# Optimization experiments

Hardware: AMD Instinct MI355X
Metric: run time of the kernel (lower is better)

Reference implementation:

```python
import jax, jax.numpy as jnp
import numpy as np

N_NODES = 50000
N_EDGES = 65536
D_NODE = 1024
D_HID = 1024


def setup_inputs() -> dict:
    key = jax.random.key(0)
    k1, k2, k3, k4, k5 = jax.random.split(key, 5)
    node_feats = jax.random.normal(k1, (N_NODES, D_NODE), dtype=jnp.float32)
    src = jax.random.randint(k2, (N_EDGES,), 0, N_NODES, dtype=jnp.int64)
    dst = jax.random.randint(k3, (N_EDGES,), 0, N_NODES, dtype=jnp.int64)
    # MLP([2048, 1024, 1024]) with ReLU between layers, bias, no BN, no dropout
    W1 = jax.random.normal(k4, (2 * D_NODE, D_HID), dtype=jnp.float32) * (1.0 / np.sqrt(2 * D_NODE))
    b1 = jnp.zeros((D_HID,), dtype=jnp.float32)
    W2 = jax.random.normal(k5, (D_HID, D_HID), dtype=jnp.float32) * (1.0 / np.sqrt(D_HID))
    b2 = jnp.zeros((D_HID,), dtype=jnp.float32)
    return {"node_feats": node_feats, "src": src, "dst": dst,
            "W1": W1, "b1": b1, "W2": W2, "b2": b2}


def reference(node_feats, src, dst, W1, b1, W2, b2):
    # gather per-edge src/dst node features and concat: [E, 2d]
    feat = jnp.concatenate([node_feats[src], node_feats[dst]], axis=1)
    # edge MLP: Linear -> ReLU -> Linear
    h = jax.nn.relu(feat @ W1 + b1)
    e_f = h @ W2 + b2  # [E, D_HID]
    return e_f
```

## Files before the change

### kernel.cpp

```cpp
#include <hip/hip_runtime.h>
#include <stdint.h>
#include <stddef.h>

typedef unsigned short u16;
typedef __bf16 bf16_t;
typedef bf16_t bf16x8 __attribute__((ext_vector_type(8)));
typedef float f32x4 __attribute__((ext_vector_type(4)));
typedef u16 u16x4 __attribute__((ext_vector_type(4)));

#define N_NODES 50000
#define N_EDGES 65536
#define D_NODE 1024
#define D_HID 1024

#define BM 256
#define BK 64
#define BUFE (BM * BK)
#define LDS_BYTES (4 * BUFE * 2)


__device__ __forceinline__ u16 f2bf(float f) {
  union { float f; uint32_t u; } v; v.f = f;
  uint32_t u = v.u;
  u += 0x7FFF + ((u >> 16) & 1);
  return (u16)(u >> 16);
}

typedef __attribute__((address_space(1))) const void GV;
typedef __attribute__((address_space(3))) void LV;

__device__ __forceinline__ void gll16(const void* g, void* lds_wave_base) {
  __builtin_amdgcn_global_load_lds((GV*)g, (LV*)lds_wave_base, 16, 0, 0);
}


__global__ void detect_i64_kernel(const int* __restrict__ src, int* __restrict__ flag) {
  if (threadIdx.x == 0 && blockIdx.x == 0) {
    int o = 0;
    for (int i = 1; i < 32; i += 2) o |= src[i];
    *flag = (o == 0) ? 1 : 0;
  }
}

__global__ void cvt_bf16_kernel(const float* __restrict__ in, u16* __restrict__ out, size_t n4) {
  size_t i = (size_t)blockIdx.x * blockDim.x + threadIdx.x;
  if (i >= n4) return;
  float4 v = reinterpret_cast<const float4*>(in)[i];
  u16x4 o;
  o.x = f2bf(v.x); o.y = f2bf(v.y); o.z = f2bf(v.z); o.w = f2bf(v.w);
  reinterpret_cast<u16x4*>(out)[i] = o;
}

__global__ void transpose_cvt_kernel(const float* __restrict__ in, u16* __restrict__ out,
                                     int K, int N) {
  __shared__ float tile[32][33];
  int n0 = blockIdx.x * 32, k0 = blockIdx.y * 32;
  int tx = threadIdx.x, ty = threadIdx.y;
  #pragma unroll
  for (int i = ty; i < 32; i += 8)
    tile[i][tx] = in[(size_t)(k0 + i) * N + (n0 + tx)];
  __syncthreads();
  #pragma unroll
  for (int i = ty; i < 32; i += 8)
    out[(size_t)(n0 + i) * K + (k0 + tx)] = f2bf(tile[tx][i]);
}


template <bool FIRST>
__device__ __forceinline__ void gemm_body(const u16* __restrict__ Abf,
                                          const int* __restrict__ src,
                                          const int* __restrict__ dst,
                                          const int* __restrict__ is64p,
                                          const u16* __restrict__ Bt,
                                          const float* __restrict__ bias,
                                          u16* __restrict__ hout,
                                          float* __restrict__ fout,
                                          const int K) {
  extern __shared__ __align__(16) u16 lds[];
  u16* const ldsA = lds;
  u16* const ldsB = lds + 2 * BUFE;

  const int t = threadIdx.x;
  const int lane = t & 63;
  const int wave = t >> 6;

  const int b = blockIdx.x;
  const int wgid = (b & 7) * 128 + (b >> 3);
  const int bm = (wgid >> 2) * BM;
  const int bn = (wgid & 3) * BM;

  const int wm = (wave >> 2) * 128;
  const int wn = (wave & 3) * 64;

  const int srow = t >> 3;
  const int kswz = (((t & 7) ^ (srow & 7)) << 3);
  const int stoff = wave * 512;

  const u16* ap[4];
  const u16* ad[4];
  const u16* bp[4];
  if constexpr (FIRST) {
    const int is64 = *is64p;
    #pragma unroll
    for (int q = 0; q < 4; ++q) {
      const int e = bm + q * 64 + srow;
      const int s = is64 ? src[2 * e] : src[e];
      const int d = is64 ? dst[2 * e] : dst[e];
      ap[q] = Abf + (size_t)s * D_NODE + kswz;
      ad[q] = Abf + (size_t)d * D_NODE + kswz;
    }
  } else {
    #pragma unroll
    for (int q = 0; q < 4; ++q) {
      ap[q] = Abf + (size_t)(bm + q * 64 + srow) * K + kswz;
      ad[q] = nullptr;
    }
  }
  #pragma unroll
  for (int q = 0; q < 4; ++q)
    bp[q] = Bt + (size_t)(bn + q * 64 + srow) * K + kswz;

  auto stageA = [&](int buf, int q, int u) {
    const u16* g;
    if constexpr (FIRST) {
      g = (u < (D_NODE / BK)) ? (ap[q] + u * BK) : (ad[q] + (u - D_NODE / BK) * BK);
    } else {
      g = ap[q] + u * BK;
    }
    gll16(g, ldsA + buf * BUFE + q * 4096 + stoff);
  };
  auto stageB = [&](int buf, int q, int u) {
    gll16(bp[q] + u * BK, ldsB + buf * BUFE + q * 4096 + stoff);
  };
  auto stageGroup = [&](int buf, int u) {
    stageA(buf, 0, u); stageA(buf, 1, u); stageA(buf, 2, u); stageA(buf, 3, u);
    stageB(buf, 0, u); stageB(buf, 1, u); stageB(buf, 2, u); stageB(buf, 3, u);
  };

  const int lm = lane & 15;
  const int kq8 = ((lane >> 4) & 3) << 3;
  const int swzr = (lm & 7) << 3;
  const int kb0 = kq8 ^ swzr;
  const int kb1 = (32 + kq8) ^ swzr;
  const int arow = (wm + lm) * BK;
  const int brow = (wn + lm) * BK;

  f32x4 acc[8][4] = {};

  const int NT = K / BK;

  stageGroup(0, 0);
  stageGroup(1, 1);
  asm volatile("s_waitcnt vmcnt(8)" ::: "memory");
  __builtin_amdgcn_s_barrier();

  for (int u = 0; u < NT; ++u) {
    const int cb = u & 1;
    const u16* As_c = ldsA + cb * BUFE;
    const u16* Bs_c = ldsB + cb * BUFE;

    bf16x8 aq[4], ar[4], bq[4], br[4];

    #pragma unroll
    for (int j = 0; j < 4; ++j)
      bq[j] = *reinterpret_cast<const bf16x8*>(Bs_c + brow + j * 1024 + kb0);
    #pragma unroll
    for (int i = 0; i < 4; ++i)
      aq[i] = *reinterpret_cast<const bf16x8*>(As_c + arow + i * 1024 + kb0);
    #pragma unroll
    for (int i = 0; i < 4; ++i)
      ar[i] = *reinterpret_cast<const bf16x8*>(As_c + arow + (i + 4) * 1024 + kb0);

    __builtin_amdgcn_s_setprio(1);
    #pragma unroll
    for (int i = 0; i < 4; ++i)
      #pragma unroll
      for (int j = 0; j < 4; ++j)
        acc[i][j] = __builtin_amdgcn_mfma_f32_16x16x32_bf16(aq[i], bq[j], acc[i][j], 0, 0, 0);
    __builtin_amdgcn_s_setprio(0);

    #pragma unroll
    for (int j = 0; j < 4; ++j)
      br[j] = *reinterpret_cast<const bf16x8*>(Bs_c + brow + j * 1024 + kb1);
    bf16x8 aq2[4];
    #pragma unroll
    for (int i = 0; i < 4; ++i)
      aq2[i] = *reinterpret_cast<const bf16x8*>(As_c + arow + i * 1024 + kb1);
    bf16x8 ar2[4];
    #pragma unroll
    for (int i = 0; i < 4; ++i)
      ar2[i] = *reinterpret_cast<const bf16x8*>(As_c + arow + (i + 4) * 1024 + kb1);

    __builtin_amdgcn_s_setprio(1);
    #pragma unroll
    for (int i = 0; i < 4; ++i)
      #pragma unroll
      for (int j = 0; j < 4; ++j)
        acc[i + 4][j] = __builtin_amdgcn_mfma_f32_16x16x32_bf16(ar[i], bq[j], acc[i + 4][j], 0, 0, 0);
    __builtin_amdgcn_s_setprio(0);

    asm volatile("s_waitcnt lgkmcnt(0)" ::: "memory");
    __builtin_amdgcn_sched_barrier(0);
    __builtin_amdgcn_s_barrier();
    __builtin_amdgcn_sched_barrier(0);

    if (u + 2 < NT) stageGroup(cb, u + 2);

    __builtin_amdgcn_s_setprio(1);
    #pragma unroll
    for (int i = 0; i < 4; ++i)
      #pragma unroll
      for (int j = 0; j < 4; ++j)
        acc[i][j] = __builtin_amdgcn_mfma_f32_16x16x32_bf16(aq2[i], br[j], acc[i][j], 0, 0, 0);
    #pragma unroll
    for (int i = 0; i < 4; ++i)
      #pragma unroll
      for (int j = 0; j < 4; ++j)
        acc[i + 4][j] = __builtin_amdgcn_mfma_f32_16x16x32_bf16(ar2[i], br[j], acc[i + 4][j], 0, 0, 0);
    __builtin_amdgcn_s_setprio(0);

    if (u + 2 < NT)      asm volatile("s_waitcnt vmcnt(8)" ::: "memory");
    else if (u + 1 < NT) asm volatile("s_waitcnt vmcnt(0)" ::: "memory");
    __builtin_amdgcn_s_barrier();
  }

  const int rq = ((lane >> 4) & 3) * 4;
  #pragma unroll
  for (int j = 0; j < 4; ++j) {
    const int n = bn + wn + 16 * j + lm;
    const float bj = bias[n];
    #pragma unroll
    for (int i = 0; i < 8; ++i) {
      const int m0 = bm + wm + 16 * i + rq;
      f32x4 c = acc[i][j];
      #pragma unroll
      for (int rr = 0; rr < 4; ++rr) {
        float vv = c[rr] + bj;
        if (FIRST) {
          vv = fmaxf(vv, 0.0f);
          hout[(size_t)(m0 + rr) * D_HID + n] = f2bf(vv);
        } else {
          fout[(size_t)(m0 + rr) * D_HID + n] = vv;
        }
      }
    }
  }
}

__launch_bounds__(512, 2)
__global__ void gemm1_kernel(const u16* __restrict__ Abf, const int* __restrict__ src,
                             const int* __restrict__ dst, const int* __restrict__ is64p,
                             const u16* __restrict__ Bt, const float* __restrict__ bias,
                             u16* __restrict__ hout) {
  gemm_body<true>(Abf, src, dst, is64p, Bt, bias, hout, nullptr, 2 * D_NODE);
}

__launch_bounds__(512, 2)
__global__ void gemm2_kernel(const u16* __restrict__ Abf, const u16* __restrict__ Bt,
                             const float* __restrict__ bias, float* __restrict__ fout) {
  gemm_body<false>(Abf, nullptr, nullptr, nullptr, Bt, bias, nullptr, fout, D_HID);
}


extern "C" void kernel_launch(void* const* d_in, const int* in_sizes, int n_in,
                              void* d_out, int out_size, void* d_ws, size_t ws_size,
                              hipStream_t stream) {
  const float* node_feats = (const float*)d_in[0];
  const int*   src        = (const int*)d_in[1];
  const int*   dst        = (const int*)d_in[2];
  const float* W1         = (const float*)d_in[3];
  const float* b1         = (const float*)d_in[4];
  const float* W2         = (const float*)d_in[5];
  const float* b2         = (const float*)d_in[6];
  float* out = (float*)d_out;

  u16* ws = (u16*)d_ws;
  const size_t NODE_E = (size_t)N_NODES * D_NODE;
  u16* node_bf = ws;
  u16* W1T = node_bf + NODE_E;
  u16* W2T = W1T + (size_t)2048 * 1024;
  u16* h   = W2T + (size_t)1024 * 1024;
  int* flag = (int*)(h + (size_t)N_EDGES * D_HID);

  static bool attr_set = false;
  if (!attr_set) {
    hipFuncSetAttribute(reinterpret_cast<const void*>(&gemm1_kernel),
                        hipFuncAttributeMaxDynamicSharedMemorySize, LDS_BYTES);
    hipFuncSetAttribute(reinterpret_cast<const void*>(&gemm2_kernel),
                        hipFuncAttributeMaxDynamicSharedMemorySize, LDS_BYTES);
    attr_set = true;
  }

  detect_i64_kernel<<<1, 64, 0, stream>>>(src, flag);

  cvt_bf16_kernel<<<(unsigned)(NODE_E / 4 / 256), 256, 0, stream>>>(node_feats, node_bf, NODE_E / 4);

  transpose_cvt_kernel<<<dim3(1024 / 32, 2048 / 32), dim3(32, 8), 0, stream>>>(W1, W1T, 2048, 1024);
  transpose_cvt_kernel<<<dim3(1024 / 32, 1024 / 32), dim3(32, 8), 0, stream>>>(W2, W2T, 1024, 1024);

  gemm1_kernel<<<1024, 512, LDS_BYTES, stream>>>(node_bf, src, dst, flag, W1T, b1, h);

  gemm2_kernel<<<1024, 512, LDS_BYTES, stream>>>(h, W2T, b2, out);
}
```

Baseline: 804.5 us.

## Switch GEMMs to 4-wave blocks with 128x128 per-wave tiles and simpler double buffering

Each workgroup now runs 256 threads (4 waves), and each wave computes a 128x128 output tile with an 8x8 accumulator array instead of 128x64 with 8 waves. The hand-tuned two-stage prefetch with split barriers and setprio is replaced by a plain double buffer: prefetch the next tile at the top of the loop, then __syncthreads at the end. Global addressing switches to 32-bit byte offsets to save registers. The larger register tile raises MFMA reuse per LDS load, but it needs many more VGPRs, and occupancy drops to one block per CU, so latency hiding relies on the single prefetch stage.

```diff
diff --git a/kernel.cpp b/kernel.cpp
--- a/kernel.cpp
+++ b/kernel.cpp
@@ -89,144 +89,108 @@
   const int bm = (wgid >> 2) * BM;
   const int bn = (wgid & 3) * BM;
 
-  const int wm = (wave >> 2) * 128;
-  const int wn = (wave & 3) * 64;
-
-  const int srow = t >> 3;
-  const int kswz = (((t & 7) ^ (srow & 7)) << 3);
-  const int stoff = wave * 512;
-
-  const u16* ap[4];
-  const u16* ad[4];
-  const u16* bp[4];
+  const int wm = (wave >> 1) * 128;
+  const int wn = (wave & 1) * 128;
+
+  const int srb = t >> 3;
+  const int kswz = (((t & 7) ^ (srb & 7)) << 3);
+
+  uint32_t aoff[8], doff[8], boff[8];
   if constexpr (FIRST) {
     const int is64 = *is64p;
     #pragma unroll
-    for (int q = 0; q < 4; ++q) {
-      const int e = bm + q * 64 + srow;
+    for (int qr = 0; qr < 8; ++qr) {
+      const int row = qr * 32 + srb;
+      const int e = bm + row;
       const int s = is64 ? src[2 * e] : src[e];
       const int d = is64 ? dst[2 * e] : dst[e];
-      ap[q] = Abf + (size_t)s * D_NODE + kswz;
-      ad[q] = Abf + (size_t)d * D_NODE + kswz;
+      aoff[qr] = ((uint32_t)s * D_NODE + (uint32_t)kswz) * 2u;
+      doff[qr] = ((uint32_t)d * D_NODE + (uint32_t)kswz) * 2u;
+      boff[qr] = ((uint32_t)(bn + row) * (uint32_t)K + (uint32_t)kswz) * 2u;
     }
   } else {
     #pragma unroll
-    for (int q = 0; q < 4; ++q) {
-      ap[q] = Abf + (size_t)(bm + q * 64 + srow) * K + kswz;
-      ad[q] = nullptr;
-    }
-  }
-  #pragma unroll
-  for (int q = 0; q < 4; ++q)
-    bp[q] = Bt + (size_t)(bn + q * 64 + srow) * K + kswz;
-
-  auto stageA = [&](int buf, int q, int u) {
-    const u16* g;
+    for (int qr = 0; qr < 8; ++qr) {
+      const int row = qr * 32 + srb;
+      aoff[qr] = ((uint32_t)(bm + row) * (uint32_t)K + (uint32_t)kswz) * 2u;
+      boff[qr] = ((uint32_t)(bn + row) * (uint32_t)K + (uint32_t)kswz) * 2u;
+    }
+  }
+
+  auto stageA = [&](int buf, int qr, int u) {
+    uint32_t off;
     if constexpr (FIRST) {
-      g = (u < (D_NODE / BK)) ? (ap[q] + u * BK) : (ad[q] + (u - D_NODE / BK) * BK);
+      off = (u < D_NODE / BK) ? aoff[qr] + (uint32_t)(u * BK * 2)
+                              : doff[qr] + (uint32_t)((u - D_NODE / BK) * BK * 2);
     } else {
-      g = ap[q] + u * BK;
-    }
-    gll16(g, ldsA + buf * BUFE + q * 4096 + stoff);
+      off = aoff[qr] + (uint32_t)(u * BK * 2);
+    }
+    gll16((const char*)Abf + off, ldsA + buf * BUFE + qr * 2048 + wave * 512);
   };
-  auto stageB = [&](int buf, int q, int u) {
-    gll16(bp[q] + u * BK, ldsB + buf * BUFE + q * 4096 + stoff);
+  auto stageB = [&](int buf, int qr, int u) {
+    gll16((const char*)Bt + (boff[qr] + (uint32_t)(u * BK * 2)),
+          ldsB + buf * BUFE + qr * 2048 + wave * 512);
   };
   auto stageGroup = [&](int buf, int u) {
-    stageA(buf, 0, u); stageA(buf, 1, u); stageA(buf, 2, u); stageA(buf, 3, u);
-    stageB(buf, 0, u); stageB(buf, 1, u); stageB(buf, 2, u); stageB(buf, 3, u);
+    #pragma unroll
+    for (int qr = 0; qr < 8; ++qr) stageA(buf, qr, u);
+    #pragma unroll
+    for (int qr = 0; qr < 8; ++qr) stageB(buf, qr, u);
   };
 
   const int lm = lane & 15;
-  const int kq8 = ((lane >> 4) & 3) << 3;
+  const int qw = lane >> 4;
+  const int kq8 = qw << 3;
   const int swzr = (lm & 7) << 3;
   const int kb0 = kq8 ^ swzr;
   const int kb1 = (32 + kq8) ^ swzr;
   const int arow = (wm + lm) * BK;
   const int brow = (wn + lm) * BK;
 
-  f32x4 acc[8][4] = {};
+  f32x4 acc[8][8] = {};
 
   const int NT = K / BK;
 
   stageGroup(0, 0);
-  stageGroup(1, 1);
-  asm volatile("s_waitcnt vmcnt(8)" ::: "memory");
-  __builtin_amdgcn_s_barrier();
+  __syncthreads();
 
   for (int u = 0; u < NT; ++u) {
     const int cb = u & 1;
     const u16* As_c = ldsA + cb * BUFE;
     const u16* Bs_c = ldsB + cb * BUFE;
 
-    bf16x8 aq[4], ar[4], bq[4], br[4];
-
-    #pragma unroll
-    for (int j = 0; j < 4; ++j)
-      bq[j] = *reinterpret_cast<const bf16x8*>(Bs_c + brow + j * 1024 + kb0);
-    #pragma unroll
-    for (int i = 0; i < 4; ++i)
-      aq[i] = *reinterpret_cast<const bf16x8*>(As_c + arow + i * 1024 + kb0);
-    #pragma unroll
-    for (int i = 0; i < 4; ++i)
-      ar[i] = *reinterpret_cast<const bf16x8*>(As_c + arow + (i + 4) * 1024 + kb0);
-
-    __builtin_amdgcn_s_setprio(1);
-    #pragma unroll
-    for (int i = 0; i < 4; ++i)
+    if (u + 1 < NT) stageGroup(cb ^ 1, u + 1);
+
+    bf16x8 bf0[8];
+    #pragma unroll
+    for (int j = 0; j < 8; ++j)
+      bf0[j] = *reinterpret_cast<const bf16x8*>(Bs_c + brow + j * 1024 + kb0);
+    #pragma unroll
+    for (int i = 0; i < 8; ++i) {
+      bf16x8 a = *reinterpret_cast<const bf16x8*>(As_c + arow + i * 1024 + kb0);
       #pragma unroll
-      for (int j = 0; j < 4; ++j)
-        acc[i][j] = __builtin_amdgcn_mfma_f32_16x16x32_bf16(aq[i], bq[j], acc[i][j], 0, 0, 0);
-    __builtin_amdgcn_s_setprio(0);
-
-    #pragma unroll
-    for (int j = 0; j < 4; ++j)
-      br[j] = *reinterpret_cast<const bf16x8*>(Bs_c + brow + j * 1024 + kb1);
-    bf16x8 aq2[4];
-    #pragma unroll
-    for (int i = 0; i < 4; ++i)
-      aq2[i] = *reinterpret_cast<const bf16x8*>(As_c + arow + i * 1024 + kb1);
-    bf16x8 ar2[4];
-    #pragma unroll
-    for (int i = 0; i < 4; ++i)
-      ar2[i] = *reinterpret_cast<const bf16x8*>(As_c + arow + (i + 4) * 1024 + kb1);
-
-    __builtin_amdgcn_s_setprio(1);
-    #pragma unroll
-    for (int i = 0; i < 4; ++i)
+      for (int j = 0; j < 8; ++j)
+        acc[i][j] = __builtin_amdgcn_mfma_f32_16x16x32_bf16(a, bf0[j], acc[i][j], 0, 0, 0);
+    }
+
+    bf16x8 bf1[8];
+    #pragma unroll
+    for (int j = 0; j < 8; ++j)
+      bf1[j] = *reinterpret_cast<const bf16x8*>(Bs_c + brow + j * 1024 + kb1);
+    #pragma unroll
+    for (int i = 0; i < 8; ++i) {
+      bf16x8 a = *reinterpret_cast<const bf16x8*>(As_c + arow + i * 1024 + kb1);
       #pragma unroll
-      for (int j = 0; j < 4; ++j)
-        acc[i + 4][j] = __builtin_amdgcn_mfma_f32_16x16x32_bf16(ar[i], bq[j], acc[i + 4][j], 0, 0, 0);
-    __builtin_amdgcn_s_setprio(0);
-
-    asm volatile("s_waitcnt lgkmcnt(0)" ::: "memory");
-    __builtin_amdgcn_sched_barrier(0);
-    __builtin_amdgcn_s_barrier();
-    __builtin_amdgcn_sched_barrier(0);
-
-    if (u + 2 < NT) stageGroup(cb, u + 2);
-
-    __builtin_amdgcn_s_setprio(1);
-    #pragma unroll
-    for (int i = 0; i < 4; ++i)
-      #pragma unroll
-      for (int j = 0; j < 4; ++j)
-        acc[i][j] = __builtin_amdgcn_mfma_f32_16x16x32_bf16(aq2[i], br[j], acc[i][j], 0, 0, 0);
-    #pragma unroll
-    for (int i = 0; i < 4; ++i)
-      #pragma unroll
-      for (int j = 0; j < 4; ++j)
-        acc[i + 4][j] = __builtin_amdgcn_mfma_f32_16x16x32_bf16(ar2[i], br[j], acc[i + 4][j], 0, 0, 0);
-    __builtin_amdgcn_s_setprio(0);
-
-    if (u + 2 < NT)      asm volatile("s_waitcnt vmcnt(8)" ::: "memory");
-    else if (u + 1 < NT) asm volatile("s_waitcnt vmcnt(0)" ::: "memory");
-    __builtin_amdgcn_s_barrier();
-  }
-
-  const int rq = ((lane >> 4) & 3) * 4;
+      for (int j = 0; j < 8; ++j)
+        acc[i][j] = __builtin_amdgcn_mfma_f32_16x16x32_bf16(a, bf1[j], acc[i][j], 0, 0, 0);
+    }
+
+    __syncthreads();
+  }
+
+  const int rq = qw * 4;
   #pragma unroll
-  for (int j = 0; j < 4; ++j) {
+  for (int j = 0; j < 8; ++j) {
     const int n = bn + wn + 16 * j + lm;
     const float bj = bias[n];
     #pragma unroll
@@ -247,7 +211,7 @@
   }
 }
 
-__launch_bounds__(512, 2)
+__launch_bounds__(256, 1)
 __global__ void gemm1_kernel(const u16* __restrict__ Abf, const int* __restrict__ src,
                              const int* __restrict__ dst, const int* __restrict__ is64p,
                              const u16* __restrict__ Bt, const float* __restrict__ bias,
@@ -255,7 +219,7 @@
   gemm_body<true>(Abf, src, dst, is64p, Bt, bias, hout, nullptr, 2 * D_NODE);
 }
 
-__launch_bounds__(512, 2)
+__launch_bounds__(256, 1)
 __global__ void gemm2_kernel(const u16* __restrict__ Abf, const u16* __restrict__ Bt,
                              const float* __restrict__ bias, float* __restrict__ fout) {
   gemm_body<false>(Abf, nullptr, nullptr, nullptr, Bt, bias, nullptr, fout, D_HID);
@@ -298,7 +262,7 @@
   transpose_cvt_kernel<<<dim3(1024 / 32, 2048 / 32), dim3(32, 8), 0, stream>>>(W1, W1T, 2048, 1024);
   transpose_cvt_kernel<<<dim3(1024 / 32, 1024 / 32), dim3(32, 8), 0, stream>>>(W2, W2T, 1024, 1024);
 
-  gemm1_kernel<<<1024, 512, LDS_BYTES, stream>>>(node_bf, src, dst, flag, W1T, b1, h);
-
-  gemm2_kernel<<<1024, 512, LDS_BYTES, stream>>>(h, W2T, b2, out);
-}
+  gemm1_kernel<<<1024, 256, LDS_BYTES, stream>>>(node_bf, src, dst, flag, W1T, b1, h);
+
+  gemm2_kernel<<<1024, 256, LDS_BYTES, stream>>>(h, W2T, b2, out);
+}
```

After: 993.9 us. +23.5%, slower.
